# Performance work log

Hardware: AMD Instinct MI355X
Metric: run time of the kernel (lower is better)

Reference implementation:

```python
import jax, jax.numpy as jnp
import numpy as np

EPS = 1e-5
SLOPE = 0.01  # torch LeakyReLU default negative slope


def _bn(h, gamma, beta):
    # BatchNorm1d in training mode: biased batch statistics over the batch dim
    mu = jnp.mean(h, axis=0)
    var = jnp.var(h, axis=0)
    return gamma * (h - mu) * jax.lax.rsqrt(var + EPS) + beta


def _leaky(h):
    return jnp.where(h >= 0, h, SLOPE * h)


def _forward(x, adj, w_gc1, b_gc1, w_gc2, b_gc2, w_gc3, b_gc3,
             w_fc0, b_fc0, g_fc0, be_fc0, w_fc1, b_fc1, g_fc1, be_fc1, w_fc2, b_fc2):
    B, S, Fp1 = x.shape
    F = Fp1 - 1
    N = adj.shape[0]
    # --- scatter: build per-sample node features from first S-1 timesteps ---
    sids = x[:, :S - 1, -2].astype(jnp.int32)                                   # [B,S-1]
    feats = jnp.concatenate([x[:, :S - 1, :-2], x[:, :S - 1, -1:]], axis=-1)    # [B,S-1,F]
    X = jnp.zeros((B, N, F), x.dtype).at[jnp.arange(B)[:, None], sids].set(feats)
    # --- symmetric-normalized adjacency with self loops: D^-1/2 (A+I) D^-1/2 ---
    A = adj + jnp.eye(N, dtype=adj.dtype)
    d = jax.lax.rsqrt(jnp.sum(A, axis=1))
    Ahat = d[:, None] * A * d[None, :]                                          # [N,N]
    # --- fc0 branch on last-timestep features ---
    h0 = _leaky(_bn(x[:, -1, :-2] @ w_fc0 + b_fc0, g_fc0, be_fc0))              # [B,FH]
    # --- 3-layer GCN: relu(Ahat @ X @ W + b) ---
    X = jax.nn.relu(jnp.einsum('mn,bnf->bmf', Ahat, X) @ w_gc1 + b_gc1)
    X = jax.nn.relu(jnp.einsum('mn,bnf->bmf', Ahat, X) @ w_gc2 + b_gc2)
    X = jax.nn.relu(jnp.einsum('mn,bnf->bmf', Ahat, X) @ w_gc3 + b_gc3)         # [B,N,GH]
    # --- gather station-specific rows ---
    sid_last = x[:, -1, -2].astype(jnp.int32)                                   # [B]
    g = X[jnp.arange(B), sid_last]                                              # [B,GH]
    # --- fusion MLP head ---
    h = jnp.concatenate([h0, g], axis=1)
    h = _leaky(_bn(h @ w_fc1 + b_fc1, g_fc1, be_fc1))
    return jax.nn.sigmoid(h @ w_fc2 + b_fc2)                                    # [B,1]


def setup_inputs() -> dict:
    B, N, S, F = 128, 2000, 64, 16
    GH, FH = 512, 512
    key = jax.random.key(0)
    ks = jax.random.split(key, 12)
    x = jax.random.normal(ks[0], (B, S, F + 1), dtype=jnp.float32)
    # station-id column (-2): unique ids per sample so scatter writes are unambiguous
    perms = jax.vmap(lambda k: jax.random.permutation(k, N)[:S])(jax.random.split(ks[1], B))  # [B,S]
    x = x.at[:, :, -2].set(perms.astype(jnp.float32))
    # random symmetric 0/1 adjacency, avg degree ~32
    adj = (jax.random.uniform(ks[2], (N, N)) < (32.0 / N)).astype(jnp.float32)
    adj = jnp.maximum(adj, adj.T)

    def lin(k, i, o):
        kw, kb = jax.random.split(k)
        bound = 1.0 / np.sqrt(i)
        w = jax.random.uniform(kw, (i, o), jnp.float32, -bound, bound)
        b = jax.random.uniform(kb, (o,), jnp.float32, -bound, bound)
        return w, b

    w_gc1, b_gc1 = lin(ks[3], F, GH // 2)
    w_gc2, b_gc2 = lin(ks[4], GH // 2, GH // 2)
    w_gc3, b_gc3 = lin(ks[5], GH // 2, GH)
    w_fc0, b_fc0 = lin(ks[6], F - 1, FH)
    w_fc1, b_fc1 = lin(ks[7], GH + FH, FH)
    w_fc2, b_fc2 = lin(ks[8], FH, 1)
    g_fc0 = jnp.ones((FH,), jnp.float32)
    be_fc0 = jnp.zeros((FH,), jnp.float32)
    g_fc1 = jnp.ones((FH,), jnp.float32)
    be_fc1 = jnp.zeros((FH,), jnp.float32)
    return dict(x=x, adj=adj, w_gc1=w_gc1, b_gc1=b_gc1, w_gc2=w_gc2, b_gc2=b_gc2,
                w_gc3=w_gc3, b_gc3=b_gc3, w_fc0=w_fc0, b_fc0=b_fc0, g_fc0=g_fc0, be_fc0=be_fc0,
                w_fc1=w_fc1, b_fc1=b_fc1, g_fc1=g_fc1, be_fc1=be_fc1, w_fc2=w_fc2, b_fc2=b_fc2)


def reference(x, adj, w_gc1, b_gc1, w_gc2, b_gc2, w_gc3, b_gc3, w_fc0, b_fc0, g_fc0, be_fc0,
              w_fc1, b_fc1, g_fc1, be_fc1, w_fc2, b_fc2):
    return _forward(x, adj, w_gc1, b_gc1, w_gc2, b_gc2, w_gc3, b_gc3,
                    w_fc0, b_fc0, g_fc0, be_fc0, w_fc1, b_fc1, g_fc1, be_fc1, w_fc2, b_fc2)
```

## Files before the change

### kernel.cpp

```cpp
#include <hip/hip_runtime.h>
#include <hip/hip_bf16.h>

typedef __hip_bfloat16 bf16;
typedef short s8v __attribute__((ext_vector_type(8)));
typedef float f4v __attribute__((ext_vector_type(4)));
typedef float f2v __attribute__((ext_vector_type(2)));

#define B   128
#define N   2000
#define S   64
#define CAP 128
#define JT  16
#define JG  8
#define XROW 1088

__device__ inline ushort bfb(float v) {
    union { __hip_bfloat16 h; ushort u; } c; c.h = __float2bfloat16(v); return c.u;
}

__global__ __launch_bounds__(256) void k_prep0(const float* __restrict__ adj,
                                               float* __restrict__ d,
                                               const float* __restrict__ w1,
                                               const float* __restrict__ w2,
                                               uint4* __restrict__ wf1,
                                               uint4* __restrict__ wf2) {
    int blk = blockIdx.x;
    if (blk < N) {
        int m = blk;
        const float* row = adj + (size_t)m * N;
        float s = 0.f;
        for (int c = threadIdx.x; c < N; c += 256) s += row[c];
        for (int o = 32; o > 0; o >>= 1) s += __shfl_down(s, o);
        __shared__ float red[4];
        int wave = threadIdx.x >> 6;
        if ((threadIdx.x & 63) == 0) red[wave] = s;
        __syncthreads();
        if (threadIdx.x == 0)
            d[m] = rsqrtf(red[0] + red[1] + red[2] + red[3] + 1.0f);
    } else {
        int blk2 = blk - N;
        if (blk2 < 4) {
            int e = blk2 * 256 + threadIdx.x;
            int ct = e >> 6, l = e & 63;
            int kg = l >> 4, ch = ct * 16 + (l & 15);
            ushort h[8];
#pragma unroll
            for (int j = 0; j < 8; ++j) {
                int f = kg * 8 + j;
                h[j] = (f < 16) ? bfb(w1[f * 256 + ch]) : (ushort)0;
            }
            uint4 r;
            r.x = h[0] | ((uint)h[1] << 16);
            r.y = h[2] | ((uint)h[3] << 16);
            r.z = h[4] | ((uint)h[5] << 16);
            r.w = h[6] | ((uint)h[7] << 16);
            wf1[e] = r;
        } else {
            int e = (blk2 - 4) * 256 + threadIdx.x;
            int l = e & 63;
            int kc = (e >> 6) & 7;
            int nt = e >> 9;
            int col = l & 15, kg = l >> 4;
            ushort h[8];
#pragma unroll
            for (int i = 0; i < 8; ++i) {
                int k = kc * 32 + kg * 8 + i;
                h[i] = bfb(w2[k * 256 + nt * 16 + col]);
            }
            uint4 r;
            r.x = h[0] | ((uint)h[1] << 16);
            r.y = h[2] | ((uint)h[3] << 16);
            r.z = h[4] | ((uint)h[5] << 16);
            r.w = h[6] | ((uint)h[7] << 16);
            wf2[e] = r;
        }
    }
}

__global__ __launch_bounds__(256) void k_prep1(const float* __restrict__ adj,
                                               const float* __restrict__ d,
                                               const float* __restrict__ x,
                                               int* __restrict__ cnt,
                                               int* __restrict__ idx,
                                               float* __restrict__ val,
                                               int* __restrict__ sid,
                                               int* __restrict__ sid_last,
                                               uint4* __restrict__ feA) {
    int blk = blockIdx.x;
    if (blk < 500) {
        int m = blk * 4 + (threadIdx.x >> 6);
        int lane = threadIdx.x & 63;
        const float* row = adj + (size_t)m * N;
        float dm = d[m];
        int base = 0;
        for (int c0 = 0; c0 < N; c0 += 64) {
            int c = c0 + lane;
            float a = 0.f;
            if (c < N) { a = row[c]; if (c == m) a += 1.0f; }
            bool pred = (a != 0.f);
            unsigned long long mask = __ballot(pred);
            int pos = base + __popcll(mask & ((1ull << lane) - 1ull));
            if (pred && pos < CAP) {
                idx[m * CAP + pos] = c;
                val[m * CAP + pos] = dm * d[c] * a;
            }
            base += (int)__popcll(mask);
        }
        if (lane == 0) cnt[m] = base < CAP ? base : CAP;
    } else {
        int b = blk - 500, tid = threadIdx.x;
        const float* xb = x + (size_t)b * XROW;
        __shared__ float dss_sh[63];
        __shared__ float fe_sh[64][16];
        if (tid < S - 1) {
            int s_ = (int)xb[tid * 17 + 15];
            sid[b * (S - 1) + tid] = s_;
            dss_sh[tid] = d[s_];
        }
        if (tid == S - 1) sid_last[b] = (int)xb[(S - 1) * 17 + 15];
        if (tid >= 240 && tid < 256) fe_sh[63][tid - 240] = 0.f;
        __syncthreads();
        for (int i = tid; i < (S - 1) * 16; i += 256) {
            int t = i >> 4, f = i & 15;
            fe_sh[t][f] = dss_sh[t] * xb[t * 17 + (f < 15 ? f : 16)];
        }
        __syncthreads();
        if (tid < 128) {
            int kc = tid >> 6, l = tid & 63;
            int f = l & 15, tg = l >> 4;
            ushort h[8];
#pragma unroll
            for (int j = 0; j < 8; ++j)
                h[j] = bfb(fe_sh[kc * 32 + tg * 8 + j][f]);
            uint4 r;
            r.x = h[0] | ((uint)h[1] << 16);
            r.y = h[2] | ((uint)h[3] << 16);
            r.z = h[4] | ((uint)h[5] << 16);
            r.w = h[6] | ((uint)h[7] << 16);
            feA[(b * 2 + kc) * 64 + l] = r;
        }
    }
}

__global__ __launch_bounds__(256) void k_x1(const float* __restrict__ adj,
                                            const float* __restrict__ d,
                                            const int* __restrict__ sid,
                                            const uint4* __restrict__ feA,
                                            const uint4* __restrict__ wfrag,
                                            const float* __restrict__ b1,
                                            unsigned char* __restrict__ X1) {
    __shared__ int sv[64];
    __shared__ __align__(16) ushort Ylds[64][40];
    __shared__ float b1s[256];
    __shared__ __align__(16) uint Xs[4][16][68];
    int b = blockIdx.y, p0 = blockIdx.x * 64, tid = threadIdx.x;
    b1s[tid] = b1[tid];
    if (tid < 63) sv[tid] = sid[b * 63 + tid];
    if (tid == 63) sv[63] = 0;
    __syncthreads();

    int l = tid & 63, wv = tid >> 6;
    int lm = l & 15, lg = l >> 4;
    int pt = p0 + wv * 16;
    int pcol = pt + lm;
    bool pv = (pcol < N);
    int pc = pv ? pcol : 0;

    s8v a1_0 = *(const s8v*)&feA[(b * 2 + 0) * 64 + l];
    s8v a1_1 = *(const s8v*)&feA[(b * 2 + 1) * 64 + l];

    int ss[16];
#pragma unroll
    for (int q = 0; q < 16; ++q)
        ss[q] = sv[(q >> 3) * 32 + lg * 8 + (q & 7)];
    float av[16];
#pragma unroll
    for (int q = 0; q < 16; ++q)
        av[q] = adj[(size_t)ss[q] * N + pc];
#pragma unroll
    for (int q = 0; q < 16; ++q) {
        av[q] = pv ? av[q] : 0.f;
        if (pcol == ss[q]) av[q] += 1.0f;
    }
    ushort h[16];
#pragma unroll
    for (int q = 0; q < 16; ++q) h[q] = bfb(av[q]);
    s8v b1f, b2f;
    {
        uint4 t0, t1;
        t0.x = h[0] | ((uint)h[1] << 16);  t0.y = h[2] | ((uint)h[3] << 16);
        t0.z = h[4] | ((uint)h[5] << 16);  t0.w = h[6] | ((uint)h[7] << 16);
        t1.x = h[8] | ((uint)h[9] << 16);  t1.y = h[10] | ((uint)h[11] << 16);
        t1.z = h[12] | ((uint)h[13] << 16); t1.w = h[14] | ((uint)h[15] << 16);
        b1f = *(s8v*)&t0; b2f = *(s8v*)&t1;
    }
    f4v D1 = (f4v){0.f, 0.f, 0.f, 0.f};
    D1 = __builtin_amdgcn_mfma_f32_16x16x32_bf16(a1_0, b1f, D1, 0, 0, 0);
    D1 = __builtin_amdgcn_mfma_f32_16x16x32_bf16(a1_1, b2f, D1, 0, 0, 0);
    float dp = d[pc] * (pv ? 1.f : 0.f);
    uint2 pk;
    pk.x = bfb(D1[0] * dp) | ((uint)bfb(D1[1] * dp) << 16);
    pk.y = bfb(D1[2] * dp) | ((uint)bfb(D1[3] * dp) << 16);
    *(uint2*)&Ylds[wv * 16 + lm][lg * 4] = pk;
    *(uint2*)&Ylds[wv * 16 + lm][16 + lg * 4] = make_uint2(0u, 0u);
    __syncthreads();

    s8v yf = *(const s8v*)&Ylds[wv * 16 + lm][lg * 8];
    f4v acc2[16];
#pragma unroll
    for (int ct = 0; ct < 16; ++ct) acc2[ct] = (f4v){0.f, 0.f, 0.f, 0.f};
#pragma unroll
    for (int ct = 0; ct < 16; ++ct) {
        s8v wfv = *(const s8v*)&wfrag[ct * 64 + l];
        acc2[ct] = __builtin_amdgcn_mfma_f32_16x16x32_bf16(wfv, yf, acc2[ct], 0, 0, 0);
    }
#pragma unroll
    for (int ct = 0; ct < 16; ++ct) {
        float4 bz = *(float4*)&b1s[ct * 16 + lg * 4];
        float v0 = acc2[ct][0] + bz.x; v0 = v0 > 0.f ? v0 : 0.f;
        float v1 = acc2[ct][1] + bz.y; v1 = v1 > 0.f ? v1 : 0.f;
        float v2 = acc2[ct][2] + bz.z; v2 = v2 > 0.f ? v2 : 0.f;
        float v3 = acc2[ct][3] + bz.w; v3 = v3 > 0.f ? v3 : 0.f;
        uint pk8 = (uint)__builtin_amdgcn_cvt_pk_fp8_f32(v0, v1, 0, false);
        pk8 = (uint)__builtin_amdgcn_cvt_pk_fp8_f32(v2, v3, (int)pk8, true);
        Xs[wv][lm][ct * 4 + lg] = pk8;
    }
    __syncthreads();
    {
        uint4* dstb = (uint4*)((uint*)X1 + ((size_t)b * N + p0 + wv * 16) * 64);
#pragma unroll
        for (int i = 0; i < 4; ++i) {
            int g = l + 64 * i;
            int r = g >> 4, c4 = g & 15;
            if (p0 + wv * 16 + r < N)
                dstb[g] = *(uint4*)&Xs[wv][r][c4 * 4];
        }
    }
}

__global__ __launch_bounds__(256) void k_gather(const int* __restrict__ cnt,
                                                const int* __restrict__ idxA,
                                                const float* __restrict__ valA,
                                                const int* __restrict__ sid_last,
                                                const unsigned char* __restrict__ X1,
                                                bf16* __restrict__ aggG) {
    __shared__ int   nns[JG];
    __shared__ int   ncn_s[JG];
    __shared__ int   nidx[JG][CAP];
    __shared__ float nval[JG][CAP];
    int b = blockIdx.y, j0 = blockIdx.x * JG, tid = threadIdx.x;
    int m = sid_last[b];
    int cj = cnt[m];
    if (tid < JG) {
        int j = j0 + tid;
        int n = idxA[m * CAP + (j < cj ? j : 0)];
        nns[tid] = n;
        ncn_s[tid] = (j < cj) ? cnt[n] : 0;
    }
    __syncthreads();
    for (int i = tid; i < JG * CAP; i += 256) {
        int jj = i >> 7, k = i & (CAP - 1);
        int n = nns[jj], c = ncn_s[jj];
        nidx[jj][k] = (k < c) ? idxA[n * CAP + k] : 0;
        nval[jj][k] = (k < c) ? valA[n * CAP + k] : 0.f;
    }
    __syncthreads();
    int lane = tid & 63;
    int w = __builtin_amdgcn_readfirstlane(tid >> 6);
    int la = w * 2, lb = la + 1;
    const uint* X1bl = (const uint*)X1 + (size_t)b * N * 64 + lane;
    int cA = ncn_s[la], cB = ncn_s[lb];
    int cmax = cA > cB ? cA : cB;
    float aA0 = 0.f, aA1 = 0.f, aA2 = 0.f, aA3 = 0.f;
    float aB0 = 0.f, aB1 = 0.f, aB2 = 0.f, aB3 = 0.f;
    if (cmax > 0) {
        uint uA0, uA1, uA2, uA3, uB0, uB1, uB2, uB3;
        float vA0, vA1, vA2, vA3, vB0, vB1, vB2, vB3;
        uA0 = X1bl[(size_t)nidx[la][0] * 64]; vA0 = nval[la][0];
        uA1 = X1bl[(size_t)nidx[la][1] * 64]; vA1 = nval[la][1];
        uA2 = X1bl[(size_t)nidx[la][2] * 64]; vA2 = nval[la][2];
        uA3 = X1bl[(size_t)nidx[la][3] * 64]; vA3 = nval[la][3];
        uB0 = X1bl[(size_t)nidx[lb][0] * 64]; vB0 = nval[lb][0];
        uB1 = X1bl[(size_t)nidx[lb][1] * 64]; vB1 = nval[lb][1];
        uB2 = X1bl[(size_t)nidx[lb][2] * 64]; vB2 = nval[lb][2];
        uB3 = X1bl[(size_t)nidx[lb][3] * 64]; vB3 = nval[lb][3];
        int c4 = (cmax + 3) & ~3;
        for (int k = 0; k < c4; k += 4) {
            uint cA0 = uA0, cA1 = uA1, cA2 = uA2, cA3 = uA3;
            uint cB0 = uB0, cB1 = uB1, cB2 = uB2, cB3 = uB3;
            float wA0 = vA0, wA1 = vA1, wA2 = vA2, wA3 = vA3;
            float wB0 = vB0, wB1 = vB1, wB2 = vB2, wB3 = vB3;
            int k4 = k + 4; k4 = k4 < CAP ? k4 : CAP - 1;
            int k5 = k + 5; k5 = k5 < CAP ? k5 : CAP - 1;
            int k6 = k + 6; k6 = k6 < CAP ? k6 : CAP - 1;
            int k7 = k + 7; k7 = k7 < CAP ? k7 : CAP - 1;
            uA0 = X1bl[(size_t)nidx[la][k4] * 64]; vA0 = nval[la][k4];
            uA1 = X1bl[(size_t)nidx[la][k5] * 64]; vA1 = nval[la][k5];
            uA2 = X1bl[(size_t)nidx[la][k6] * 64]; vA2 = nval[la][k6];
            uA3 = X1bl[(size_t)nidx[la][k7] * 64]; vA3 = nval[la][k7];
            uB0 = X1bl[(size_t)nidx[lb][k4] * 64]; vB0 = nval[lb][k4];
            uB1 = X1bl[(size_t)nidx[lb][k5] * 64]; vB1 = nval[lb][k5];
            uB2 = X1bl[(size_t)nidx[lb][k6] * 64]; vB2 = nval[lb][k6];
            uB3 = X1bl[(size_t)nidx[lb][k7] * 64]; vB3 = nval[lb][k7];
            f2v lo, hi;
            lo = __builtin_amdgcn_cvt_pk_f32_fp8((int)cA0, false);
            hi = __builtin_amdgcn_cvt_pk_f32_fp8((int)cA0, true);
            aA0 += wA0 * lo.x; aA1 += wA0 * lo.y; aA2 += wA0 * hi.x; aA3 += wA0 * hi.y;
            lo = __builtin_amdgcn_cvt_pk_f32_fp8((int)cA1, false);
            hi = __builtin_amdgcn_cvt_pk_f32_fp8((int)cA1, true);
            aA0 += wA1 * lo.x; aA1 += wA1 * lo.y; aA2 += wA1 * hi.x; aA3 += wA1 * hi.y;
            lo = __builtin_amdgcn_cvt_pk_f32_fp8((int)cA2, false);
            hi = __builtin_amdgcn_cvt_pk_f32_fp8((int)cA2, true);
            aA0 += wA2 * lo.x; aA1 += wA2 * lo.y; aA2 += wA2 * hi.x; aA3 += wA2 * hi.y;
            lo = __builtin_amdgcn_cvt_pk_f32_fp8((int)cA3, false);
            hi = __builtin_amdgcn_cvt_pk_f32_fp8((int)cA3, true);
            aA0 += wA3 * lo.x; aA1 += wA3 * lo.y; aA2 += wA3 * hi.x; aA3 += wA3 * hi.y;
            lo = __builtin_amdgcn_cvt_pk_f32_fp8((int)cB0, false);
            hi = __builtin_amdgcn_cvt_pk_f32_fp8((int)cB0, true);
            aB0 += wB0 * lo.x; aB1 += wB0 * lo.y; aB2 += wB0 * hi.x; aB3 += wB0 * hi.y;
            lo = __builtin_amdgcn_cvt_pk_f32_fp8((int)cB1, false);
            hi = __builtin_amdgcn_cvt_pk_f32_fp8((int)cB1, true);
            aB0 += wB1 * lo.x; aB1 += wB1 * lo.y; aB2 += wB1 * hi.x; aB3 += wB1 * hi.y;
            lo = __builtin_amdgcn_cvt_pk_f32_fp8((int)cB2, false);
            hi = __builtin_amdgcn_cvt_pk_f32_fp8((int)cB2, true);
            aB0 += wB2 * lo.x; aB1 += wB2 * lo.y; aB2 += wB2 * hi.x; aB3 += wB2 * hi.y;
            lo = __builtin_amdgcn_cvt_pk_f32_fp8((int)cB3, false);
            hi = __builtin_amdgcn_cvt_pk_f32_fp8((int)cB3, true);
            aB0 += wB3 * lo.x; aB1 += wB3 * lo.y; aB2 += wB3 * hi.x; aB3 += wB3 * hi.y;
        }
    }
    uint2 pkA, pkB;
    pkA.x = bfb(aA0) | ((uint)bfb(aA1) << 16);
    pkA.y = bfb(aA2) | ((uint)bfb(aA3) << 16);
    pkB.x = bfb(aB0) | ((uint)bfb(aB1) << 16);
    pkB.y = bfb(aB2) | ((uint)bfb(aB3) << 16);
    uint2* ag = (uint2*)aggG;
    ag[((size_t)b * CAP + j0 + la) * 64 + lane] = pkA;
    ag[((size_t)b * CAP + j0 + lb) * 64 + lane] = pkB;
}

__global__ __launch_bounds__(256) void k_x2g(const int* __restrict__ cnt,
                                             const int* __restrict__ sid_last,
                                             const float* __restrict__ valA,
                                             const bf16* __restrict__ aggG,
                                             const uint4* __restrict__ w2f,
                                             const float* __restrict__ b2,
                                             float* __restrict__ gaggP) {
    __shared__ ushort agg[JT][264];
    __shared__ float vs[JT];
    int b = blockIdx.y, j0 = blockIdx.x * JT, tid = threadIdx.x;
    int m = sid_last[b];
    int cj = cnt[m];
    if (j0 >= cj) return;
    int nj = cj - j0; if (nj > JT) nj = JT;
    if (tid < JT) vs[tid] = (tid < nj) ? valA[m * CAP + j0 + tid] : 0.f;
    {
        const uint4* src = (const uint4*)(aggG + ((size_t)b * CAP + j0) * 256);
        for (int i = tid; i < 512; i += 256) {
            int row = i >> 5, col = i & 31;
            *(uint4*)&agg[row][col * 8] = src[i];
        }
    }
    __syncthreads();
    int lane = tid & 63;
    int w = __builtin_amdgcn_readfirstlane(tid >> 6);
    int col = lane & 15, rg = lane >> 4;
    s8v af[8];
#pragma unroll
    for (int kc = 0; kc < 8; ++kc)
        af[kc] = *(const s8v*)&agg[col][kc * 32 + rg * 8];
    float* outp = gaggP + ((size_t)b * 8 + blockIdx.x) * 256;
#pragma unroll
    for (int t = 0; t < 4; ++t) {
        int nt = w * 4 + t;
        f4v acc = (f4v){0.f, 0.f, 0.f, 0.f};
#pragma unroll
        for (int kc = 0; kc < 8; ++kc) {
            s8v bf = *(const s8v*)&w2f[(nt * 8 + kc) * 64 + lane];
            acc = __builtin_amdgcn_mfma_f32_16x16x32_bf16(af[kc], bf, acc, 0, 0, 0);
        }
        float bv = b2[nt * 16 + col];
        float p = 0.f;
#pragma unroll
        for (int i = 0; i < 4; ++i) {
            float vv = acc[i] + bv;
            vv = vv > 0.f ? vv : 0.f;
            p += vs[rg * 4 + i] * vv;
        }
        p += __shfl_xor(p, 16);
        p += __shfl_xor(p, 32);
        if (lane < 16) outp[nt * 16 + col] = p;
    }
}

__global__ __launch_bounds__(256) void k_gmm(const int* __restrict__ cnt,
                                             const int* __restrict__ sid_last,
                                             const float* __restrict__ gaggP,
                                             const float* __restrict__ w3,
                                             const float* __restrict__ b3,
                                             float* __restrict__ g) {
    int b = blockIdx.x, ot = blockIdx.y, tid = threadIdx.x;
    __shared__ float h[256];
    {
        int m = sid_last[b];
        int cj = cnt[m];
        int nq = (cj + JT - 1) / JT;
        const float* p = gaggP + (size_t)b * 8 * 256 + tid;
        float s = 0.f;
        for (int q = 0; q < nq; ++q) s += p[q * 256];
        h[tid] = s;
    }
    __syncthreads();
    int q  = tid & 31;
    int kg = tid >> 5;
    const float4* w4 = (const float4*)w3;
    int wq = ot * 32 + q;
    float4 acc = {0.f, 0.f, 0.f, 0.f};
    for (int k = kg * 32; k < kg * 32 + 32; ++k) {
        float hk = h[k];
        float4 w = w4[(size_t)k * 128 + wq];
        acc.x += hk * w.x; acc.y += hk * w.y; acc.z += hk * w.z; acc.w += hk * w.w;
    }
    __shared__ float4 red[8][32];
    red[kg][q] = acc;
    __syncthreads();
    if (tid < 32) {
        float4 s = red[0][tid];
#pragma unroll
        for (int gr = 1; gr < 8; ++gr) {
            float4 r = red[gr][tid];
            s.x += r.x; s.y += r.y; s.z += r.z; s.w += r.w;
        }
        int ob = ot * 128 + tid * 4;
        s.x += b3[ob];     s.x = s.x > 0.f ? s.x : 0.f;
        s.y += b3[ob + 1]; s.y = s.y > 0.f ? s.y : 0.f;
        s.z += b3[ob + 2]; s.z = s.z > 0.f ? s.z : 0.f;
        s.w += b3[ob + 3]; s.w = s.w > 0.f ? s.w : 0.f;
        *(float4*)&g[(size_t)b * 512 + ob] = s;
    }
}

__global__ __launch_bounds__(256) void k_fc0s(const float* __restrict__ x,
                                              const float* __restrict__ w0,
                                              const float* __restrict__ b0,
                                              float* __restrict__ hp0,
                                              float* __restrict__ mu0,
                                              float* __restrict__ rstd0) {
    int tid = threadIdx.x;
    int c = tid >> 7, b = tid & 127;
    int o = blockIdx.x * 2 + c;
    const float* xr = x + (size_t)b * XROW + (S - 1) * 17;
    float acc = b0[o];
#pragma unroll
    for (int f = 0; f < 15; ++f) acc += xr[f] * w0[f * 512 + o];
    hp0[b * 512 + o] = acc;
    float s = acc, s2 = acc * acc;
    for (int off = 32; off > 0; off >>= 1) {
        s += __shfl_down(s, off);
        s2 += __shfl_down(s2, off);
    }
    __shared__ float rs[4], rs2[4];
    int wv = tid >> 6;
    if ((tid & 63) == 0) { rs[wv] = s; rs2[wv] = s2; }
    __syncthreads();
    if ((tid & 127) == 0) {
        float S1 = rs[c * 2] + rs[c * 2 + 1];
        float S2 = rs2[c * 2] + rs2[c * 2 + 1];
        float m = S1 * (1.f / B);
        float var = S2 * (1.f / B) - m * m;
        mu0[o] = m;
        rstd0[o] = rsqrtf(var + 1e-5f);
    }
}

__global__ __launch_bounds__(256) void k_bn1w(const float* __restrict__ h,
                                              float* __restrict__ mu,
                                              float* __restrict__ rstd) {
    int tid = threadIdx.x;
    int o = blockIdx.x * 32 + (tid & 31);
    int bg = tid >> 5;
    float s = 0.f, s2 = 0.f;
    for (int b = bg * 16; b < bg * 16 + 16; ++b) {
        float v = h[b * 512 + o];
        s += v; s2 += v * v;
    }
    __shared__ float rs[8][32], rs2[8][32];
    rs[bg][tid & 31] = s; rs2[bg][tid & 31] = s2;
    __syncthreads();
    if (tid < 32) {
        float S1 = 0.f, S2 = 0.f;
#pragma unroll
        for (int g2 = 0; g2 < 8; ++g2) { S1 += rs[g2][tid]; S2 += rs2[g2][tid]; }
        float m = S1 * (1.f / B);
        float var = S2 * (1.f / B) - m * m;
        mu[blockIdx.x * 32 + tid] = m;
        rstd[blockIdx.x * 32 + tid] = rsqrtf(var + 1e-5f);
    }
}

__global__ __launch_bounds__(256) void k_fc1(const float* __restrict__ hp0,
                                             const float* __restrict__ mu0,
                                             const float* __restrict__ rstd0,
                                             const float* __restrict__ gam,
                                             const float* __restrict__ bet,
                                             const float* __restrict__ gbuf,
                                             const float* __restrict__ w1,
                                             const float* __restrict__ b1,
                                             float* __restrict__ hp1) {
    int b = blockIdx.x, ot = blockIdx.y, tid = threadIdx.x;
    __shared__ float h[1024];
    for (int o = tid; o < 512; o += 256) {
        float v = hp0[b * 512 + o];
        v = gam[o] * (v - mu0[o]) * rstd0[o] + bet[o];
        h[o] = v >= 0.f ? v : 0.01f * v;
        h[512 + o] = gbuf[(size_t)b * 512 + o];
    }
    __syncthreads();
    int q  = tid & 31;
    int kg = tid >> 5;
    const float4* w4 = (const float4*)w1;
    int wq = ot * 32 + q;
    float4 acc = {0.f, 0.f, 0.f, 0.f};
    for (int k = kg * 128; k < kg * 128 + 128; ++k) {
        float hk = h[k];
        float4 w = w4[(size_t)k * 128 + wq];
        acc.x += hk * w.x; acc.y += hk * w.y; acc.z += hk * w.z; acc.w += hk * w.w;
    }
    __shared__ float4 red[8][32];
    red[kg][q] = acc;
    __syncthreads();
    if (tid < 32) {
        float4 s = red[0][tid];
#pragma unroll
        for (int gr = 1; gr < 8; ++gr) {
            float4 r = red[gr][tid];
            s.x += r.x; s.y += r.y; s.z += r.z; s.w += r.w;
        }
        int ob = ot * 128 + tid * 4;
        s.x += b1[ob]; s.y += b1[ob + 1]; s.z += b1[ob + 2]; s.w += b1[ob + 3];
        *(float4*)&hp1[b * 512 + ob] = s;
    }
}

__global__ __launch_bounds__(64) void k_out(const float* __restrict__ hp1,
                                            const float* __restrict__ mu1,
                                            const float* __restrict__ rstd1,
                                            const float* __restrict__ gam,
                                            const float* __restrict__ bet,
                                            const float* __restrict__ w2,
                                            const float* __restrict__ b2,
                                            float* __restrict__ out) {
    int b = blockIdx.x, lane = threadIdx.x;
    float acc = 0.f;
    for (int o = lane; o < 512; o += 64) {
        float v = hp1[b * 512 + o];
        v = gam[o] * (v - mu1[o]) * rstd1[o] + bet[o];
        v = v >= 0.f ? v : 0.01f * v;
        acc += v * w2[o];
    }
    for (int off = 32; off > 0; off >>= 1) acc += __shfl_down(acc, off);
    if (lane == 0) out[b] = 1.f / (1.f + expf(-(acc + b2[0])));
}

static inline size_t align256(size_t x) { return (x + 255) & ~(size_t)255; }

extern "C" void kernel_launch(void* const* d_in, const int* in_sizes, int n_in,
                              void* d_out, int out_size, void* d_ws, size_t ws_size,
                              hipStream_t stream) {
    const float* x     = (const float*)d_in[0];
    const float* adj   = (const float*)d_in[1];
    const float* w_gc1 = (const float*)d_in[2];
    const float* b_gc1 = (const float*)d_in[3];
    const float* w_gc2 = (const float*)d_in[4];
    const float* b_gc2 = (const float*)d_in[5];
    const float* w_gc3 = (const float*)d_in[6];
    const float* b_gc3 = (const float*)d_in[7];
    const float* w_fc0 = (const float*)d_in[8];
    const float* b_fc0 = (const float*)d_in[9];
    const float* g_fc0 = (const float*)d_in[10];
    const float* be_fc0= (const float*)d_in[11];
    const float* w_fc1 = (const float*)d_in[12];
    const float* b_fc1 = (const float*)d_in[13];
    const float* g_fc1 = (const float*)d_in[14];
    const float* be_fc1= (const float*)d_in[15];
    const float* w_fc2 = (const float*)d_in[16];
    const float* b_fc2 = (const float*)d_in[17];

    char* wsp = (char*)d_ws;
    size_t off = 0;
    auto alloc = [&](size_t bytes) { void* p = wsp + off; off = align256(off + bytes); return p; };
    float* d_deg   = (float*)alloc((size_t)N * 4);
    int*   sid     = (int*)  alloc((size_t)B * 63 * 4);
    int*   sidl    = (int*)  alloc((size_t)B * 4);
    uint4* feA     = (uint4*)alloc((size_t)B * 2 * 64 * 16);
    uint4* wfrag   = (uint4*)alloc((size_t)1024 * 16);
    uint4* w2frag  = (uint4*)alloc((size_t)8192 * 16);
    int*   csr_cnt = (int*)  alloc((size_t)N * 4);
    int*   csr_idx = (int*)  alloc((size_t)N * CAP * 4);
    float* csr_val = (float*)alloc((size_t)N * CAP * 4);
    unsigned char* X1 = (unsigned char*)alloc((size_t)B * N * 256);
    bf16*  aggG    = (bf16*) alloc((size_t)B * CAP * 256 * 2);
    float* gaggP   = (float*)alloc((size_t)B * 8 * 256 * 4);
    float* gbuf    = (float*)alloc((size_t)B * 512 * 4);
    float* hp0     = (float*)alloc((size_t)B * 512 * 4);
    float* mu0     = (float*)alloc(512 * 4);
    float* rstd0   = (float*)alloc(512 * 4);
    float* hp1     = (float*)alloc((size_t)B * 512 * 4);
    float* mu1     = (float*)alloc(512 * 4);
    float* rstd1   = (float*)alloc(512 * 4);

    k_prep0 <<<N + 36, 256, 0, stream>>>(adj, d_deg, w_gc1, w_gc2, wfrag, w2frag);
    k_prep1 <<<500 + B, 256, 0, stream>>>(adj, d_deg, x, csr_cnt, csr_idx, csr_val, sid, sidl, feA);
    k_x1    <<<dim3(32, B), 256, 0, stream>>>(adj, d_deg, sid, feA, wfrag, b_gc1, X1);
    k_gather<<<dim3(CAP / JG, B), 256, 0, stream>>>(csr_cnt, csr_idx, csr_val, sidl, X1, aggG);
    k_x2g   <<<dim3(CAP / JT, B), 256, 0, stream>>>(csr_cnt, sidl, csr_val, aggG, w2frag, b_gc2, gaggP);
    k_gmm   <<<dim3(B, 4), 256, 0, stream>>>(csr_cnt, sidl, gaggP, w_gc3, b_gc3, gbuf);
    k_fc0s  <<<256, 256, 0, stream>>>(x, w_fc0, b_fc0, hp0, mu0, rstd0);
    k_fc1   <<<dim3(B, 4), 256, 0, stream>>>(hp0, mu0, rstd0, g_fc0, be_fc0, gbuf, w_fc1, b_fc1, hp1);
    k_bn1w  <<<16, 256, 0, stream>>>(hp1, mu1, rstd1);
    k_out   <<<B, 64, 0, stream>>>(hp1, mu1, rstd1, g_fc1, be_fc1, w_fc2, b_fc2, (float*)d_out);
}
```

Before: 124.7 us.

## Fuse neighbor gather into layer-2 GEMM kernel and fold fc0 into prep

```diff
diff --git a/kernel.cpp b/kernel.cpp
--- a/kernel.cpp
+++ b/kernel.cpp
@@ -11,7 +11,6 @@
 #define S   64
 #define CAP 128
 #define JT  16
-#define JG  8
 #define XROW 1088
 
 __device__ inline ushort bfb(float v) {
@@ -85,7 +84,12 @@
                                                float* __restrict__ val,
                                                int* __restrict__ sid,
                                                int* __restrict__ sid_last,
-                                               uint4* __restrict__ feA) {
+                                               uint4* __restrict__ feA,
+                                               const float* __restrict__ w0,
+                                               const float* __restrict__ b0,
+                                               float* __restrict__ hp0,
+                                               float* __restrict__ mu0,
+                                               float* __restrict__ rstd0) {
     int blk = blockIdx.x;
     if (blk < 500) {
         int m = blk * 4 + (threadIdx.x >> 6);
@@ -107,7 +111,7 @@
             base += (int)__popcll(mask);
         }
         if (lane == 0) cnt[m] = base < CAP ? base : CAP;
-    } else {
+    } else if (blk < 500 + B) {
         int b = blk - 500, tid = threadIdx.x;
         const float* xb = x + (size_t)b * XROW;
         __shared__ float dss_sh[63];
@@ -138,6 +142,32 @@
             r.z = h[4] | ((uint)h[5] << 16);
             r.w = h[6] | ((uint)h[7] << 16);
             feA[(b * 2 + kc) * 64 + l] = r;
+        }
+    } else {
+        int tid = threadIdx.x;
+        int c = tid >> 7, b = tid & 127;
+        int o = (blk - 500 - B) * 2 + c;
+        const float* xr = x + (size_t)b * XROW + (S - 1) * 17;
+        float acc = b0[o];
+#pragma unroll
+        for (int f = 0; f < 15; ++f) acc += xr[f] * w0[f * 512 + o];
+        hp0[b * 512 + o] = acc;
+        float s = acc, s2 = acc * acc;
+        for (int off = 32; off > 0; off >>= 1) {
+            s += __shfl_down(s, off);
+            s2 += __shfl_down(s2, off);
+        }
+        __shared__ float rs[4], rs2[4];
+        int wv = tid >> 6;
+        if ((tid & 63) == 0) { rs[wv] = s; rs2[wv] = s2; }
+        __syncthreads();
+        if ((tid & 127) == 0) {
+            float S1 = rs[c * 2] + rs[c * 2 + 1];
+            float S2 = rs2[c * 2] + rs2[c * 2 + 1];
+            float m = S1 * (1.f / B);
+            float var = S2 * (1.f / B) - m * m;
+            mu0[o] = m;
+            rstd0[o] = rsqrtf(var + 1e-5f);
         }
     }
 }
@@ -238,132 +268,95 @@
     }
 }
 
-__global__ __launch_bounds__(256) void k_gather(const int* __restrict__ cnt,
-                                                const int* __restrict__ idxA,
-                                                const float* __restrict__ valA,
-                                                const int* __restrict__ sid_last,
-                                                const unsigned char* __restrict__ X1,
-                                                bf16* __restrict__ aggG) {
-    __shared__ int   nns[JG];
-    __shared__ int   ncn_s[JG];
-    __shared__ int   nidx[JG][CAP];
-    __shared__ float nval[JG][CAP];
-    int b = blockIdx.y, j0 = blockIdx.x * JG, tid = threadIdx.x;
-    int m = sid_last[b];
-    int cj = cnt[m];
-    if (tid < JG) {
-        int j = j0 + tid;
-        int n = idxA[m * CAP + (j < cj ? j : 0)];
-        nns[tid] = n;
-        ncn_s[tid] = (j < cj) ? cnt[n] : 0;
-    }
-    __syncthreads();
-    for (int i = tid; i < JG * CAP; i += 256) {
-        int jj = i >> 7, k = i & (CAP - 1);
-        int n = nns[jj], c = ncn_s[jj];
-        nidx[jj][k] = (k < c) ? idxA[n * CAP + k] : 0;
-        nval[jj][k] = (k < c) ? valA[n * CAP + k] : 0.f;
-    }
-    __syncthreads();
-    int lane = tid & 63;
-    int w = __builtin_amdgcn_readfirstlane(tid >> 6);
-    int la = w * 2, lb = la + 1;
-    const uint* X1bl = (const uint*)X1 + (size_t)b * N * 64 + lane;
-    int cA = ncn_s[la], cB = ncn_s[lb];
-    int cmax = cA > cB ? cA : cB;
-    float aA0 = 0.f, aA1 = 0.f, aA2 = 0.f, aA3 = 0.f;
-    float aB0 = 0.f, aB1 = 0.f, aB2 = 0.f, aB3 = 0.f;
-    if (cmax > 0) {
-        uint uA0, uA1, uA2, uA3, uB0, uB1, uB2, uB3;
-        float vA0, vA1, vA2, vA3, vB0, vB1, vB2, vB3;
-        uA0 = X1bl[(size_t)nidx[la][0] * 64]; vA0 = nval[la][0];
-        uA1 = X1bl[(size_t)nidx[la][1] * 64]; vA1 = nval[la][1];
-        uA2 = X1bl[(size_t)nidx[la][2] * 64]; vA2 = nval[la][2];
-        uA3 = X1bl[(size_t)nidx[la][3] * 64]; vA3 = nval[la][3];
-        uB0 = X1bl[(size_t)nidx[lb][0] * 64]; vB0 = nval[lb][0];
-        uB1 = X1bl[(size_t)nidx[lb][1] * 64]; vB1 = nval[lb][1];
-        uB2 = X1bl[(size_t)nidx[lb][2] * 64]; vB2 = nval[lb][2];
-        uB3 = X1bl[(size_t)nidx[lb][3] * 64]; vB3 = nval[lb][3];
-        int c4 = (cmax + 3) & ~3;
-        for (int k = 0; k < c4; k += 4) {
-            uint cA0 = uA0, cA1 = uA1, cA2 = uA2, cA3 = uA3;
-            uint cB0 = uB0, cB1 = uB1, cB2 = uB2, cB3 = uB3;
-            float wA0 = vA0, wA1 = vA1, wA2 = vA2, wA3 = vA3;
-            float wB0 = vB0, wB1 = vB1, wB2 = vB2, wB3 = vB3;
-            int k4 = k + 4; k4 = k4 < CAP ? k4 : CAP - 1;
-            int k5 = k + 5; k5 = k5 < CAP ? k5 : CAP - 1;
-            int k6 = k + 6; k6 = k6 < CAP ? k6 : CAP - 1;
-            int k7 = k + 7; k7 = k7 < CAP ? k7 : CAP - 1;
-            uA0 = X1bl[(size_t)nidx[la][k4] * 64]; vA0 = nval[la][k4];
-            uA1 = X1bl[(size_t)nidx[la][k5] * 64]; vA1 = nval[la][k5];
-            uA2 = X1bl[(size_t)nidx[la][k6] * 64]; vA2 = nval[la][k6];
-            uA3 = X1bl[(size_t)nidx[la][k7] * 64]; vA3 = nval[la][k7];
-            uB0 = X1bl[(size_t)nidx[lb][k4] * 64]; vB0 = nval[lb][k4];
-            uB1 = X1bl[(size_t)nidx[lb][k5] * 64]; vB1 = nval[lb][k5];
-            uB2 = X1bl[(size_t)nidx[lb][k6] * 64]; vB2 = nval[lb][k6];
-            uB3 = X1bl[(size_t)nidx[lb][k7] * 64]; vB3 = nval[lb][k7];
-            f2v lo, hi;
-            lo = __builtin_amdgcn_cvt_pk_f32_fp8((int)cA0, false);
-            hi = __builtin_amdgcn_cvt_pk_f32_fp8((int)cA0, true);
-            aA0 += wA0 * lo.x; aA1 += wA0 * lo.y; aA2 += wA0 * hi.x; aA3 += wA0 * hi.y;
-            lo = __builtin_amdgcn_cvt_pk_f32_fp8((int)cA1, false);
-            hi = __builtin_amdgcn_cvt_pk_f32_fp8((int)cA1, true);
-            aA0 += wA1 * lo.x; aA1 += wA1 * lo.y; aA2 += wA1 * hi.x; aA3 += wA1 * hi.y;
-            lo = __builtin_amdgcn_cvt_pk_f32_fp8((int)cA2, false);
-            hi = __builtin_amdgcn_cvt_pk_f32_fp8((int)cA2, true);
-            aA0 += wA2 * lo.x; aA1 += wA2 * lo.y; aA2 += wA2 * hi.x; aA3 += wA2 * hi.y;
-            lo = __builtin_amdgcn_cvt_pk_f32_fp8((int)cA3, false);
-            hi = __builtin_amdgcn_cvt_pk_f32_fp8((int)cA3, true);
-            aA0 += wA3 * lo.x; aA1 += wA3 * lo.y; aA2 += wA3 * hi.x; aA3 += wA3 * hi.y;
-            lo = __builtin_amdgcn_cvt_pk_f32_fp8((int)cB0, false);
-            hi = __builtin_amdgcn_cvt_pk_f32_fp8((int)cB0, true);
-            aB0 += wB0 * lo.x; aB1 += wB0 * lo.y; aB2 += wB0 * hi.x; aB3 += wB0 * hi.y;
-            lo = __builtin_amdgcn_cvt_pk_f32_fp8((int)cB1, false);
-            hi = __builtin_amdgcn_cvt_pk_f32_fp8((int)cB1, true);
-            aB0 += wB1 * lo.x; aB1 += wB1 * lo.y; aB2 += wB1 * hi.x; aB3 += wB1 * hi.y;
-            lo = __builtin_amdgcn_cvt_pk_f32_fp8((int)cB2, false);
-            hi = __builtin_amdgcn_cvt_pk_f32_fp8((int)cB2, true);
-            aB0 += wB2 * lo.x; aB1 += wB2 * lo.y; aB2 += wB2 * hi.x; aB3 += wB2 * hi.y;
-            lo = __builtin_amdgcn_cvt_pk_f32_fp8((int)cB3, false);
-            hi = __builtin_amdgcn_cvt_pk_f32_fp8((int)cB3, true);
-            aB0 += wB3 * lo.x; aB1 += wB3 * lo.y; aB2 += wB3 * hi.x; aB3 += wB3 * hi.y;
-        }
-    }
-    uint2 pkA, pkB;
-    pkA.x = bfb(aA0) | ((uint)bfb(aA1) << 16);
-    pkA.y = bfb(aA2) | ((uint)bfb(aA3) << 16);
-    pkB.x = bfb(aB0) | ((uint)bfb(aB1) << 16);
-    pkB.y = bfb(aB2) | ((uint)bfb(aB3) << 16);
-    uint2* ag = (uint2*)aggG;
-    ag[((size_t)b * CAP + j0 + la) * 64 + lane] = pkA;
-    ag[((size_t)b * CAP + j0 + lb) * 64 + lane] = pkB;
-}
-
-__global__ __launch_bounds__(256) void k_x2g(const int* __restrict__ cnt,
+__global__ __launch_bounds__(256) void k_gx2(const int* __restrict__ cnt,
+                                             const int* __restrict__ idxA,
+                                             const float* __restrict__ valA,
                                              const int* __restrict__ sid_last,
-                                             const float* __restrict__ valA,
-                                             const bf16* __restrict__ aggG,
+                                             const unsigned char* __restrict__ X1,
                                              const uint4* __restrict__ w2f,
                                              const float* __restrict__ b2,
                                              float* __restrict__ gaggP) {
+    __shared__ int   nidx[JT][CAP];
+    __shared__ float nval[JT][CAP];
+    __shared__ int   nns[JT];
+    __shared__ int   ncn_s[JT];
+    __shared__ float vs[JT];
     __shared__ ushort agg[JT][264];
-    __shared__ float vs[JT];
     int b = blockIdx.y, j0 = blockIdx.x * JT, tid = threadIdx.x;
     int m = sid_last[b];
     int cj = cnt[m];
     if (j0 >= cj) return;
     int nj = cj - j0; if (nj > JT) nj = JT;
-    if (tid < JT) vs[tid] = (tid < nj) ? valA[m * CAP + j0 + tid] : 0.f;
-    {
-        const uint4* src = (const uint4*)(aggG + ((size_t)b * CAP + j0) * 256);
-        for (int i = tid; i < 512; i += 256) {
-            int row = i >> 5, col = i & 31;
-            *(uint4*)&agg[row][col * 8] = src[i];
-        }
+    if (tid < JT) {
+        int j = j0 + tid;
+        int n = idxA[m * CAP + (j < cj ? j : 0)];
+        nns[tid] = n;
+        ncn_s[tid] = (j < cj) ? cnt[n] : 0;
+        vs[tid] = (tid < nj) ? valA[m * CAP + j] : 0.f;
+    }
+    __syncthreads();
+    for (int i = tid; i < JT * CAP; i += 256) {
+        int jj = i >> 7, k = i & (CAP - 1);
+        int n = nns[jj], c = ncn_s[jj];
+        nidx[jj][k] = (k < c) ? idxA[n * CAP + k] : 0;
+        nval[jj][k] = (k < c) ? valA[n * CAP + k] : 0.f;
     }
     __syncthreads();
     int lane = tid & 63;
     int w = __builtin_amdgcn_readfirstlane(tid >> 6);
+    int jbase = w * 4;
+    const uint* X1bl = (const uint*)X1 + (size_t)b * N * 64 + lane;
+    float a[4][4];
+#pragma unroll
+    for (int r = 0; r < 4; ++r)
+#pragma unroll
+        for (int c = 0; c < 4; ++c) a[r][c] = 0.f;
+    int cmax = ncn_s[jbase];
+#pragma unroll
+    for (int r = 1; r < 4; ++r) { int c = ncn_s[jbase + r]; if (c > cmax) cmax = c; }
+    if (cmax > 0) {
+        uint u0[4], u1[4]; float v0[4], v1[4];
+#pragma unroll
+        for (int r = 0; r < 4; ++r) {
+            u0[r] = X1bl[(size_t)nidx[jbase + r][0] * 64]; v0[r] = nval[jbase + r][0];
+            u1[r] = X1bl[(size_t)nidx[jbase + r][1] * 64]; v1[r] = nval[jbase + r][1];
+        }
+        int c2 = (cmax + 1) & ~1;
+        for (int k = 0; k < c2; k += 2) {
+            uint cu0[4], cu1[4]; float cv0[4], cv1[4];
+#pragma unroll
+            for (int r = 0; r < 4; ++r) {
+                cu0[r] = u0[r]; cu1[r] = u1[r]; cv0[r] = v0[r]; cv1[r] = v1[r];
+            }
+            int k2 = k + 2; k2 = k2 < CAP ? k2 : CAP - 1;
+            int k3 = k + 3; k3 = k3 < CAP ? k3 : CAP - 1;
+#pragma unroll
+            for (int r = 0; r < 4; ++r) {
+                u0[r] = X1bl[(size_t)nidx[jbase + r][k2] * 64]; v0[r] = nval[jbase + r][k2];
+                u1[r] = X1bl[(size_t)nidx[jbase + r][k3] * 64]; v1[r] = nval[jbase + r][k3];
+            }
+#pragma unroll
+            for (int r = 0; r < 4; ++r) {
+                f2v lo, hi;
+                lo = __builtin_amdgcn_cvt_pk_f32_fp8((int)cu0[r], false);
+                hi = __builtin_amdgcn_cvt_pk_f32_fp8((int)cu0[r], true);
+                a[r][0] += cv0[r] * lo.x; a[r][1] += cv0[r] * lo.y;
+                a[r][2] += cv0[r] * hi.x; a[r][3] += cv0[r] * hi.y;
+                lo = __builtin_amdgcn_cvt_pk_f32_fp8((int)cu1[r], false);
+                hi = __builtin_amdgcn_cvt_pk_f32_fp8((int)cu1[r], true);
+                a[r][0] += cv1[r] * lo.x; a[r][1] += cv1[r] * lo.y;
+                a[r][2] += cv1[r] * hi.x; a[r][3] += cv1[r] * hi.y;
+            }
+        }
+    }
+#pragma unroll
+    for (int r = 0; r < 4; ++r) {
+        uint2 pk;
+        pk.x = bfb(a[r][0]) | ((uint)bfb(a[r][1]) << 16);
+        pk.y = bfb(a[r][2]) | ((uint)bfb(a[r][3]) << 16);
+        *(uint2*)&agg[jbase + r][lane * 4] = pk;
+    }
+    __syncthreads();
     int col = lane & 15, rg = lane >> 4;
     s8v af[8];
 #pragma unroll
@@ -437,39 +430,6 @@
         s.z += b3[ob + 2]; s.z = s.z > 0.f ? s.z : 0.f;
         s.w += b3[ob + 3]; s.w = s.w > 0.f ? s.w : 0.f;
         *(float4*)&g[(size_t)b * 512 + ob] = s;
-    }
-}
-
-__global__ __launch_bounds__(256) void k_fc0s(const float* __restrict__ x,
-                                              const float* __restrict__ w0,
-                                              const float* __restrict__ b0,
-                                              float* __restrict__ hp0,
-                                              float* __restrict__ mu0,
-                                              float* __restrict__ rstd0) {
-    int tid = threadIdx.x;
-    int c = tid >> 7, b = tid & 127;
-    int o = blockIdx.x * 2 + c;
-    const float* xr = x + (size_t)b * XROW + (S - 1) * 17;
-    float acc = b0[o];
-#pragma unroll
-    for (int f = 0; f < 15; ++f) acc += xr[f] * w0[f * 512 + o];
-    hp0[b * 512 + o] = acc;
-    float s = acc, s2 = acc * acc;
-    for (int off = 32; off > 0; off >>= 1) {
-        s += __shfl_down(s, off);
-        s2 += __shfl_down(s2, off);
-    }
-    __shared__ float rs[4], rs2[4];
-    int wv = tid >> 6;
-    if ((tid & 63) == 0) { rs[wv] = s; rs2[wv] = s2; }
-    __syncthreads();
-    if ((tid & 127) == 0) {
-        float S1 = rs[c * 2] + rs[c * 2 + 1];
-        float S2 = rs2[c * 2] + rs2[c * 2 + 1];
-        float m = S1 * (1.f / B);
-        float var = S2 * (1.f / B) - m * m;
-        mu0[o] = m;
-        rstd0[o] = rsqrtf(var + 1e-5f);
     }
 }
 
@@ -599,7 +559,6 @@
     int*   csr_idx = (int*)  alloc((size_t)N * CAP * 4);
     float* csr_val = (float*)alloc((size_t)N * CAP * 4);
     unsigned char* X1 = (unsigned char*)alloc((size_t)B * N * 256);
-    bf16*  aggG    = (bf16*) alloc((size_t)B * CAP * 256 * 2);
     float* gaggP   = (float*)alloc((size_t)B * 8 * 256 * 4);
     float* gbuf    = (float*)alloc((size_t)B * 512 * 4);
     float* hp0     = (float*)alloc((size_t)B * 512 * 4);
@@ -610,12 +569,11 @@
     float* rstd1   = (float*)alloc(512 * 4);
 
     k_prep0 <<<N + 36, 256, 0, stream>>>(adj, d_deg, w_gc1, w_gc2, wfrag, w2frag);
-    k_prep1 <<<500 + B, 256, 0, stream>>>(adj, d_deg, x, csr_cnt, csr_idx, csr_val, sid, sidl, feA);
+    k_prep1 <<<500 + B + 256, 256, 0, stream>>>(adj, d_deg, x, csr_cnt, csr_idx, csr_val,
+                                                sid, sidl, feA, w_fc0, b_fc0, hp0, mu0, rstd0);
     k_x1    <<<dim3(32, B), 256, 0, stream>>>(adj, d_deg, sid, feA, wfrag, b_gc1, X1);
-    k_gather<<<dim3(CAP / JG, B), 256, 0, stream>>>(csr_cnt, csr_idx, csr_val, sidl, X1, aggG);
-    k_x2g   <<<dim3(CAP / JT, B), 256, 0, stream>>>(csr_cnt, sidl, csr_val, aggG, w2frag, b_gc2, gaggP);
+    k_gx2   <<<dim3(CAP / JT, B), 256, 0, stream>>>(csr_cnt, csr_idx, csr_val, sidl, X1, w2frag, b_gc2, gaggP);
     k_gmm   <<<dim3(B, 4), 256, 0, stream>>>(csr_cnt, sidl, gaggP, w_gc3, b_gc3, gbuf);
-    k_fc0s  <<<256, 256, 0, stream>>>(x, w_fc0, b_fc0, hp0, mu0, rstd0);
     k_fc1   <<<dim3(B, 4), 256, 0, stream>>>(hp0, mu0, rstd0, g_fc0, be_fc0, gbuf, w_fc1, b_fc1, hp1);
     k_bn1w  <<<16, 256, 0, stream>>>(hp1, mu1, rstd1);
     k_out   <<<B, 64, 0, stream>>>(hp1, mu1, rstd1, g_fc1, be_fc1, w_fc2, b_fc2, (float*)d_out);
```

After: 129.1 us. 3.5% more time.
